# Kernel optimization log

Measured on AMD Instinct MI355X. Metric: run time of the kernel, lower is better.

The kernel has to match this reference:

```python
import jax, jax.numpy as jnp
import numpy as np

CUTOFF = 8.0
NUM_G = 50
HID = 128
NUM_INTER = 3
NUM_NODES = 50000
NUM_EDGES = 1600000
NUM_GRAPHS = 128
MAX_Z = 100
LOG2 = float(np.log(2.0))


def ssp(x):
    # PyG ShiftedSoftplus
    return jax.nn.softplus(x) - LOG2


def setup_inputs() -> dict:
    key = jax.random.key(0)
    ks = jax.random.split(key, 20)
    s = 0.1
    pos = jax.random.normal(ks[0], (NUM_NODES, 3), dtype=jnp.float32) * 4.0
    edge_shift = jax.random.normal(ks[1], (NUM_EDGES, 3), dtype=jnp.float32) * 0.5
    z = jax.random.randint(ks[2], (NUM_NODES,), 0, MAX_Z, dtype=jnp.int32)
    edge_index = jax.random.randint(ks[3], (2, NUM_EDGES), 0, NUM_NODES, dtype=jnp.int32)
    batch = jnp.sort(jax.random.randint(ks[4], (NUM_NODES,), 0, NUM_GRAPHS, dtype=jnp.int32))
    emb = jax.random.normal(ks[5], (MAX_Z, HID), dtype=jnp.float32) * s
    mlp_w1 = jax.random.normal(ks[6], (NUM_INTER, NUM_G, HID), dtype=jnp.float32) * s
    mlp_b1 = jnp.zeros((NUM_INTER, HID), jnp.float32)
    mlp_w2 = jax.random.normal(ks[7], (NUM_INTER, HID, HID), dtype=jnp.float32) * s
    mlp_b2 = jnp.zeros((NUM_INTER, HID), jnp.float32)
    cf_w1 = jax.random.normal(ks[8], (NUM_INTER, HID, HID), dtype=jnp.float32) * s  # no bias (PyG lin1)
    cf_w2 = jax.random.normal(ks[9], (NUM_INTER, HID, HID), dtype=jnp.float32) * s
    cf_b2 = jnp.zeros((NUM_INTER, HID), jnp.float32)
    lin_w = jax.random.normal(ks[10], (NUM_INTER, HID, HID), dtype=jnp.float32) * s
    lin_b = jnp.zeros((NUM_INTER, HID), jnp.float32)
    head_w1 = jax.random.normal(ks[11], (HID, HID // 2), dtype=jnp.float32) * s
    head_b1 = jnp.zeros((HID // 2,), jnp.float32)
    head_w2 = jax.random.normal(ks[12], (HID // 2, 1), dtype=jnp.float32) * s
    head_b2 = jnp.zeros((1,), jnp.float32)
    return dict(pos=pos, edge_shift=edge_shift, emb=emb, mlp_w1=mlp_w1, mlp_b1=mlp_b1,
                mlp_w2=mlp_w2, mlp_b2=mlp_b2, cf_w1=cf_w1, cf_w2=cf_w2, cf_b2=cf_b2,
                lin_w=lin_w, lin_b=lin_b, head_w1=head_w1, head_b1=head_b1,
                head_w2=head_w2, head_b2=head_b2, z=z, edge_index=edge_index, batch=batch)


def reference(pos, edge_shift, emb, mlp_w1, mlp_b1, mlp_w2, mlp_b2, cf_w1, cf_w2, cf_b2,
              lin_w, lin_b, head_w1, head_b1, head_w2, head_b2, z, edge_index, batch):
    src, dst = edge_index[0], edge_index[1]
    # edge distances: pos[row] - (pos[col] + shift)
    rel = pos[src] - (pos[dst] + edge_shift)            # [E,3]
    w = jnp.linalg.norm(rel, axis=-1)                   # [E]
    # Gaussian smearing
    offset = jnp.linspace(0.0, CUTOFF, NUM_G, dtype=pos.dtype)
    coeff = -0.5 / (offset[1] - offset[0]) ** 2
    edge_attr = jnp.exp(coeff * (w[:, None] - offset) ** 2)   # [E,50]
    # cosine cutoff
    C = 0.5 * (jnp.cos(w * jnp.pi / CUTOFF) + 1.0)            # [E]
    h = emb[z]                                                # [N,128]
    for i in range(NUM_INTER):
        Wf = (ssp(edge_attr @ mlp_w1[i] + mlp_b1[i]) @ mlp_w2[i] + mlp_b2[i]) * C[:, None]  # [E,128]
        msg = (h @ cf_w1[i])[src] * Wf                   # gather-multiply  [E,128]
        agg = jax.ops.segment_sum(msg, dst, num_segments=NUM_NODES)         # scatter-sum [N,128]
        h = h + (ssp(agg @ cf_w2[i] + cf_b2[i]) @ lin_w[i] + lin_b[i])
    out_atom = ssp(h @ head_w1 + head_b1) @ head_w2 + head_b2               # [N,1]
    sums = jax.ops.segment_sum(out_atom, batch, num_segments=NUM_GRAPHS)    # [G,1]
    counts = jax.ops.segment_sum(jnp.ones((NUM_NODES, 1), out_atom.dtype), batch, num_segments=NUM_GRAPHS)
    return sums / jnp.maximum(counts, 1.0)  # mean readout; out_proj is Identity (128==128)
```

## Files before the change

kernel.cpp:

```cpp
#include <hip/hip_runtime.h>
#include <hip/hip_fp16.h>
#include <math.h>

#define NNODES  50000
#define NEDGES  1600000
#define NGRAPHS 128
#define HID     128
#define NG      50
#define NITER   3
#define TPTS    2048
#define WMAX    12.0f
#define PI_F    3.14159265358979323846f

typedef __attribute__((ext_vector_type(4))) _Float16 half4;
typedef __attribute__((ext_vector_type(4))) float   f32x4;

__device__ __forceinline__ float ssp(float x) {
    float sp = fmaxf(x, 0.0f) + log1pf(expf(-fabsf(x)));
    return sp - 0.69314718055994530942f;
}

__global__ __launch_bounds__(256) void k_init_h(const float* __restrict__ emb,
                                                const int* __restrict__ z,
                                                float* __restrict__ h,
                                                _Float16* __restrict__ hH)
{
    int idx = blockIdx.x * 256 + threadIdx.x;
    int n = idx >> 7, c = idx & 127;
    float v = emb[(z[n] << 7) + c];
    h[idx] = v;
    hH[idx] = (_Float16)v;
}

__global__ __launch_bounds__(128) void k_wt(const float* __restrict__ in,
                                            _Float16* __restrict__ out)
{
    int it = blockIdx.x >> 7, c = blockIdx.x & 127, j = threadIdx.x;
    out[(size_t)it * 16384 + c * 128 + j] = (_Float16)in[(size_t)it * 16384 + j * 128 + c];
}

__global__ __launch_bounds__(128) void k_table(const float* __restrict__ W1,
                                               const float* __restrict__ B1,
                                               const float* __restrict__ W2,
                                               const float* __restrict__ B2,
                                               float* __restrict__ table)
{
    int it = blockIdx.x / TPTS;
    int pt = blockIdx.x - it * TPTS;
    const float* W1i = W1 + (size_t)it * NG * HID;
    const float* B1i = B1 + (size_t)it * HID;
    const float* W2i = W2 + (size_t)it * HID * HID;
    const float* B2i = B2 + (size_t)it * HID;

    float w = pt * (WMAX / (float)(TPTS - 1));
    __shared__ float sEA[NG];
    __shared__ float sT1[HID];
    int k = threadIdx.x;
    if (k < NG) {
        float dx = 8.0f / 49.0f;
        float coeff = -0.5f / (dx * dx);
        float diff = w - (float)k * dx;
        sEA[k] = expf(coeff * diff * diff);
    }
    __syncthreads();
    float acc = B1i[k];
    for (int g = 0; g < NG; ++g) acc = fmaf(sEA[g], W1i[g * HID + k], acc);
    sT1[k] = ssp(acc);
    __syncthreads();
    float acc2 = B2i[k];
    for (int j = 0; j < HID; ++j) acc2 = fmaf(sT1[j], W2i[j * HID + k], acc2);
    table[(size_t)blockIdx.x * HID + k] = acc2;
}

__global__ __launch_bounds__(256) void k_tdelta(const float* __restrict__ raw,
                                                __half* __restrict__ ti)
{
    int idx = blockIdx.x * 256 + threadIdx.x;
    int c = idx & 127;
    int pt_it = idx >> 7;
    int pt = pt_it & (TPTS - 1);
    float v = raw[idx];
    float nv = (pt == TPTS - 1) ? v : raw[idx + HID];
    ti[(size_t)pt_it * 256 + c * 2]     = __float2half(v);
    ti[(size_t)pt_it * 256 + c * 2 + 1] = __float2half(nv - v);
}

__global__ __launch_bounds__(256) void k_hist(const int* __restrict__ ei,
                                              int* __restrict__ deg)
{
    int e = blockIdx.x * 256 + threadIdx.x;
    if (e >= NEDGES) return;
    atomicAdd(&deg[ei[NEDGES + e]], 1);
}

#define SCAN_T 1024
#define CHUNK  49
__global__ __launch_bounds__(SCAN_T) void k_scan(const int* __restrict__ deg,
                                                 int* __restrict__ rowptr,
                                                 int* __restrict__ cursor)
{
    int tid = threadIdx.x;
    int base = tid * CHUNK;
    int vals[CHUNK];
    int local = 0;
    #pragma unroll
    for (int i = 0; i < CHUNK; ++i) {
        int idx = base + i;
        int v = (idx < NNODES) ? deg[idx] : 0;
        vals[i] = local;
        local += v;
    }
    int lane = tid & 63, wid = tid >> 6;
    int x = local;
    #pragma unroll
    for (int off = 1; off < 64; off <<= 1) {
        int y = __shfl_up(x, off);
        if (lane >= off) x += y;
    }
    __shared__ int wsum[16];
    __shared__ int woff[17];
    if (lane == 63) wsum[wid] = x;
    __syncthreads();
    if (tid == 0) {
        int acc = 0;
        #pragma unroll
        for (int i = 0; i < 16; ++i) { woff[i] = acc; acc += wsum[i]; }
        woff[16] = acc;
    }
    __syncthreads();
    int threadExcl = woff[wid] + x - local;
    #pragma unroll
    for (int i = 0; i < CHUNK; ++i) {
        int idx = base + i;
        if (idx < NNODES) {
            int p = threadExcl + vals[i];
            rowptr[idx] = p;
            cursor[idx] = p;
        }
    }
    if (tid == SCAN_T - 1) rowptr[NNODES] = woff[16];
}

__global__ __launch_bounds__(256) void k_scatter(const int* __restrict__ ei,
                                                 const float* __restrict__ pos,
                                                 const float* __restrict__ shift,
                                                 int* __restrict__ cursor,
                                                 float2* __restrict__ rec)
{
    int e = blockIdx.x * 256 + threadIdx.x;
    if (e >= NEDGES) return;
    int s = ei[e], d = ei[NEDGES + e];
    float rx = pos[3*s+0] - (pos[3*d+0] + shift[3*e+0]);
    float ry = pos[3*s+1] - (pos[3*d+1] + shift[3*e+1]);
    float rz = pos[3*s+2] - (pos[3*d+2] + shift[3*e+2]);
    float w = sqrtf(rx*rx + ry*ry + rz*rz);
    int slot = atomicAdd(&cursor[d], 1);
    rec[slot] = make_float2(__int_as_float(s), w);
}

__device__ __forceinline__ void edge_contrib(float2 r, int lane,
                                             const __half2* __restrict__ hfH,
                                             const __half* __restrict__ tableH,
                                             float& ax, float& ay)
{
    int   s = __float_as_int(r.x);
    float w = r.y;
    const float SCALE = (float)(TPTS - 1) / WMAX;
    float t = fminf(w * SCALE, (float)(TPTS - 1));
    int i0 = (int)t; if (i0 > TPTS - 2) i0 = TPTS - 2;
    float fr = t - (float)i0;
    float C = 0.5f * (__cosf(w * (PI_F / 8.0f)) + 1.0f);
    uint2 tv = *((const uint2*)(tableH + (size_t)i0 * 256) + lane);
    __half2 hv = hfH[(size_t)s * 64 + lane];
    float2 p0 = __half22float2(*(__half2*)&tv.x);
    float2 p1 = __half22float2(*(__half2*)&tv.y);
    float2 hf2 = __half22float2(hv);
    ax = fmaf(fmaf(fr, p0.y, p0.x) * C, hf2.x, ax);
    ay = fmaf(fmaf(fr, p1.y, p1.x) * C, hf2.y, ay);
}

__global__ __launch_bounds__(256) void k_gather(const float2* __restrict__ rec,
                                                const int* __restrict__ rowptr,
                                                const __half2* __restrict__ hfH,
                                                const __half* __restrict__ tableH,
                                                __half2* __restrict__ aggH)
{
    int node = blockIdx.x * 4 + (threadIdx.x >> 6);
    int lane = threadIdx.x & 63;
    int beg = rowptr[node], end = rowptr[node + 1];
    float ax0 = 0.f, ay0 = 0.f, ax1 = 0.f, ay1 = 0.f;
    int k = beg;
    for (; k + 4 <= end; k += 4) {
        float2 r0 = rec[k];
        float2 r1 = rec[k + 1];
        float2 r2 = rec[k + 2];
        float2 r3 = rec[k + 3];
        edge_contrib(r0, lane, hfH, tableH, ax0, ay0);
        edge_contrib(r1, lane, hfH, tableH, ax1, ay1);
        edge_contrib(r2, lane, hfH, tableH, ax0, ay0);
        edge_contrib(r3, lane, hfH, tableH, ax1, ay1);
    }
    for (; k < end; ++k) {
        float2 r0 = rec[k];
        edge_contrib(r0, lane, hfH, tableH, ax0, ay0);
    }
    aggH[(size_t)node * 64 + lane] = __floats2half2_rn(ax0 + ax1, ay0 + ay1);
}

__global__ __launch_bounds__(256) void k_ngemm_mfma(const _Float16* __restrict__ hH,
                                                    const _Float16* __restrict__ Wt,
                                                    _Float16* __restrict__ outH)
{
    int tid = threadIdx.x;
    int wave = tid >> 6, l = tid & 63;
    int lr = l & 15, lg = l >> 4;
    int r0 = blockIdx.x * 64 + wave * 16;
    f32x4 acc[8];
    #pragma unroll
    for (int ct = 0; ct < 8; ++ct) acc[ct] = (f32x4){0.f, 0.f, 0.f, 0.f};
    const _Float16* aRow = hH + (size_t)(r0 + lr) * HID;
    #pragma unroll
    for (int kk = 0; kk < 8; ++kk) {
        half4 a = *(const half4*)(aRow + kk * 16 + lg * 4);
        #pragma unroll
        for (int ct = 0; ct < 8; ++ct) {
            half4 b = *(const half4*)(Wt + (size_t)(ct * 16 + lr) * HID + kk * 16 + lg * 4);
            acc[ct] = __builtin_amdgcn_mfma_f32_16x16x16f16(a, b, acc[ct], 0, 0, 0);
        }
    }
    #pragma unroll
    for (int ct = 0; ct < 8; ++ct) {
        #pragma unroll
        for (int r = 0; r < 4; ++r) {
            int row = r0 + lg * 4 + r;
            if (row < NNODES) outH[(size_t)row * HID + ct * 16 + lr] = (_Float16)acc[ct][r];
        }
    }
}

__global__ __launch_bounds__(256) void k_update_mfma(const _Float16* __restrict__ aggH,
                                                     const _Float16* __restrict__ W2t,
                                                     const float* __restrict__ B2,
                                                     const _Float16* __restrict__ Lt,
                                                     const float* __restrict__ LB,
                                                     float* __restrict__ h,
                                                     _Float16* __restrict__ hH)
{
    __shared__ _Float16 sT[64 * 128];
    int tid = threadIdx.x;
    int wave = tid >> 6, l = tid & 63;
    int lr = l & 15, lg = l >> 4;
    int r0 = blockIdx.x * 64 + wave * 16;

    f32x4 acc[8];
    #pragma unroll
    for (int ct = 0; ct < 8; ++ct) acc[ct] = (f32x4){0.f, 0.f, 0.f, 0.f};
    const _Float16* aRow = aggH + (size_t)(r0 + lr) * HID;
    #pragma unroll
    for (int kk = 0; kk < 8; ++kk) {
        half4 a = *(const half4*)(aRow + kk * 16 + lg * 4);
        #pragma unroll
        for (int ct = 0; ct < 8; ++ct) {
            half4 b = *(const half4*)(W2t + (size_t)(ct * 16 + lr) * HID + kk * 16 + lg * 4);
            acc[ct] = __builtin_amdgcn_mfma_f32_16x16x16f16(a, b, acc[ct], 0, 0, 0);
        }
    }
    #pragma unroll
    for (int ct = 0; ct < 8; ++ct) {
        #pragma unroll
        for (int r = 0; r < 4; ++r) {
            int rl = wave * 16 + lg * 4 + r;
            int col = ct * 16 + lr;
            float v = ssp(acc[ct][r] + B2[col]);
            int byte = rl * 256 + col * 2;
            byte ^= (rl & 7) << 4;
            *(_Float16*)((char*)sT + byte) = (_Float16)v;
        }
    }
    __syncthreads();
    f32x4 acc2[8];
    #pragma unroll
    for (int ct = 0; ct < 8; ++ct) acc2[ct] = (f32x4){0.f, 0.f, 0.f, 0.f};
    int rl2 = wave * 16 + lr;
    #pragma unroll
    for (int kk = 0; kk < 8; ++kk) {
        int byte = rl2 * 256 + (kk * 16 + lg * 4) * 2;
        byte ^= (rl2 & 7) << 4;
        half4 a = *(const half4*)((char*)sT + byte);
        #pragma unroll
        for (int ct = 0; ct < 8; ++ct) {
            half4 b = *(const half4*)(Lt + (size_t)(ct * 16 + lr) * HID + kk * 16 + lg * 4);
            acc2[ct] = __builtin_amdgcn_mfma_f32_16x16x16f16(a, b, acc2[ct], 0, 0, 0);
        }
    }
    #pragma unroll
    for (int ct = 0; ct < 8; ++ct) {
        #pragma unroll
        for (int r = 0; r < 4; ++r) {
            int row = r0 + lg * 4 + r;
            int col = ct * 16 + lr;
            if (row < NNODES) {
                float hv = h[(size_t)row * HID + col] + acc2[ct][r] + LB[col];
                h[(size_t)row * HID + col] = hv;
                hH[(size_t)row * HID + col] = (_Float16)hv;
            }
        }
    }
}

__global__ __launch_bounds__(512) void k_head(const float* __restrict__ h,
                                              const float* __restrict__ w1,
                                              const float* __restrict__ b1,
                                              const float* __restrict__ w2,
                                              const float* __restrict__ b2,
                                              const int* __restrict__ batch,
                                              float* __restrict__ sums_pad)
{
    __shared__ float sA[128 * 132];
    int r0 = blockIdx.x * 128;
    int tid = threadIdx.x;
    for (int idx = tid; idx < 128 * 32; idx += 512) {
        int r = idx >> 5, c4 = idx & 31;
        int row = r0 + r;
        float4 v = make_float4(0.f, 0.f, 0.f, 0.f);
        if (row < NNODES) v = *(const float4*)(h + (size_t)row * HID + c4 * 4);
        *(float4*)(&sA[r * 132 + c4 * 4]) = v;
    }
    __syncthreads();
    int tx = tid & 7, ty = tid >> 3;
    int cc = tx * 8, ee = ty * 2;
    float acc[2][8];
    {
        float4 b0 = *(const float4*)(b1 + cc);
        float4 bb = *(const float4*)(b1 + cc + 4);
        #pragma unroll
        for (int e = 0; e < 2; ++e) {
            acc[e][0]=b0.x; acc[e][1]=b0.y; acc[e][2]=b0.z; acc[e][3]=b0.w;
            acc[e][4]=bb.x; acc[e][5]=bb.y; acc[e][6]=bb.z; acc[e][7]=bb.w;
        }
    }
    #pragma unroll 4
    for (int j = 0; j < HID; ++j) {
        float a0 = sA[(ee + 0) * 132 + j];
        float a1 = sA[(ee + 1) * 132 + j];
        float4 w0 = *(const float4*)(w1 + (size_t)j * 64 + cc);
        float4 wv1 = *(const float4*)(w1 + (size_t)j * 64 + cc + 4);
        float wv[8] = {w0.x,w0.y,w0.z,w0.w,wv1.x,wv1.y,wv1.z,wv1.w};
        #pragma unroll
        for (int c = 0; c < 8; ++c) {
            acc[0][c] = fmaf(a0, wv[c], acc[0][c]);
            acc[1][c] = fmaf(a1, wv[c], acc[1][c]);
        }
    }
    float4 w2a = *(const float4*)(w2 + cc);
    float4 w2b = *(const float4*)(w2 + cc + 4);
    float w2v[8] = {w2a.x,w2a.y,w2a.z,w2a.w,w2b.x,w2b.y,w2b.z,w2b.w};
    float bias2 = b2[0];
    #pragma unroll
    for (int e = 0; e < 2; ++e) {
        float part = 0.f;
        #pragma unroll
        for (int c = 0; c < 8; ++c) part = fmaf(ssp(acc[e][c]), w2v[c], part);
        part += __shfl_down(part, 4, 8);
        part += __shfl_down(part, 2, 8);
        part += __shfl_down(part, 1, 8);
        if (tx == 0) {
            int row = r0 + ee + e;
            if (row < NNODES) {
                int b = batch[row];
                atomicAdd(&sums_pad[b * 16], part + bias2);
            }
        }
    }
}

__global__ void k_final(const float* __restrict__ sums_pad,
                        const int* __restrict__ batch,
                        float* __restrict__ out)
{
    int g = threadIdx.x;
    if (g >= NGRAPHS) return;
    int lo = 0, hi = NNODES;
    while (lo < hi) { int mid = (lo + hi) >> 1; if (batch[mid] < g) lo = mid + 1; else hi = mid; }
    int a = lo;
    lo = 0; hi = NNODES;
    while (lo < hi) { int mid = (lo + hi) >> 1; if (batch[mid] < g + 1) lo = mid + 1; else hi = mid; }
    float cnt = (float)(lo - a);
    out[g] = sums_pad[g * 16] / fmaxf(cnt, 1.0f);
}

extern "C" void kernel_launch(void* const* d_in, const int* in_sizes, int n_in,
                              void* d_out, int out_size, void* d_ws, size_t ws_size,
                              hipStream_t stream)
{
    const float* pos     = (const float*)d_in[0];
    const float* shift   = (const float*)d_in[1];
    const float* emb     = (const float*)d_in[2];
    const float* mlp_w1  = (const float*)d_in[3];
    const float* mlp_b1  = (const float*)d_in[4];
    const float* mlp_w2  = (const float*)d_in[5];
    const float* mlp_b2  = (const float*)d_in[6];
    const float* cf_w1   = (const float*)d_in[7];
    const float* cf_w2   = (const float*)d_in[8];
    const float* cf_b2   = (const float*)d_in[9];
    const float* lin_w   = (const float*)d_in[10];
    const float* lin_b   = (const float*)d_in[11];
    const float* head_w1 = (const float*)d_in[12];
    const float* head_b1 = (const float*)d_in[13];
    const float* head_w2 = (const float*)d_in[14];
    const float* head_b2 = (const float*)d_in[15];
    const int*   z       = (const int*)d_in[16];
    const int*   ei      = (const int*)d_in[17];
    const int*   batch   = (const int*)d_in[18];
    float* out = (float*)d_out;

    float* ws = (float*)d_ws;
    size_t off = 0;
    float*    h       = ws + off; off += (size_t)NNODES * HID;
    _Float16* hH      = (_Float16*)(ws + off); off += (size_t)(NNODES + 64) * HID / 2;
    _Float16* hfH     = (_Float16*)(ws + off); off += (size_t)(NNODES + 64) * HID / 2;
    _Float16* aggH    = (_Float16*)(ws + off); off += (size_t)(NNODES + 64) * HID / 2;
    float*    rawT    = ws + off; off += (size_t)3 * TPTS * HID;
    __half*   tableH  = (__half*)(ws + off); off += (size_t)3 * TPTS * HID;
    _Float16* w1t     = (_Float16*)(ws + off); off += (size_t)3 * HID * HID / 2;
    _Float16* w2t     = (_Float16*)(ws + off); off += (size_t)3 * HID * HID / 2;
    _Float16* lwt     = (_Float16*)(ws + off); off += (size_t)3 * HID * HID / 2;
    float2*   rec     = (float2*)(ws + off); off += (size_t)2 * NEDGES;
    int*      rowptr  = (int*)(ws + off); off += NNODES + 1;
    int*      deg     = (int*)(ws + off); off += NNODES;
    int*      cursor  = (int*)(ws + off); off += NNODES;
    float*    sums_pad= ws + off; off += NGRAPHS * 16;

    hipMemsetAsync(deg, 0, NNODES * sizeof(int), stream);
    hipMemsetAsync(sums_pad, 0, NGRAPHS * 16 * sizeof(float), stream);

    k_hist<<<(NEDGES + 255) / 256, 256, 0, stream>>>(ei, deg);
    k_scan<<<1, SCAN_T, 0, stream>>>(deg, rowptr, cursor);
    k_scatter<<<(NEDGES + 255) / 256, 256, 0, stream>>>(ei, pos, shift, cursor, rec);

    k_init_h<<<NNODES * HID / 256, 256, 0, stream>>>(emb, z, h, hH);
    k_table<<<3 * TPTS, 128, 0, stream>>>(mlp_w1, mlp_b1, mlp_w2, mlp_b2, rawT);
    k_tdelta<<<(3 * TPTS * HID) / 256, 256, 0, stream>>>(rawT, tableH);
    k_wt<<<3 * 128, 128, 0, stream>>>(cf_w1, w1t);
    k_wt<<<3 * 128, 128, 0, stream>>>(cf_w2, w2t);
    k_wt<<<3 * 128, 128, 0, stream>>>(lin_w, lwt);

    int gblk = (NNODES + 63) / 64;
    for (int i = 0; i < NITER; ++i) {
        k_ngemm_mfma<<<gblk, 256, 0, stream>>>(hH, w1t + (size_t)i * HID * HID, hfH);
        k_gather<<<NNODES / 4, 256, 0, stream>>>(rec, rowptr, (const __half2*)hfH,
                                                 tableH + (size_t)i * TPTS * HID * 2,
                                                 (__half2*)aggH);
        k_update_mfma<<<gblk, 256, 0, stream>>>(aggH, w2t + (size_t)i * HID * HID,
                                                cf_b2 + (size_t)i * HID,
                                                lwt + (size_t)i * HID * HID,
                                                lin_b + (size_t)i * HID, h, hH);
    }
    k_head<<<(NNODES + 127) / 128, 512, 0, stream>>>(h, head_w1, head_b1, head_w2, head_b2, batch, sums_pad);
    k_final<<<1, 128, 0, stream>>>(sums_pad, batch, out);
}
```

Before: 1.051 ms.

## Precompute per-edge table offsets, fuse next-layer GEMM into update, merge table kernels

The scatter kernel now stores a 16-byte record per edge holding the pre-scaled source offset, table offset, interpolation fraction and cutoff value in fp16. This moves the index, fraction and cosine work out of the gather kernel that runs three times. The gather uses readfirstlane scalar offsets and half2 arithmetic. The update kernel also computes the next iteration's h@cf_w1 through MFMA from its shared-memory tile, which removes two separate node-GEMM launches and their hH reload. The table kernel writes interleaved fp16 values and deltas directly, dropping the tdelta pass. In exchange the edge record doubles in size, raising gather read traffic, and fp16 math adds rounding.

```diff
diff --git a/kernel.cpp b/kernel.cpp
--- a/kernel.cpp
+++ b/kernel.cpp
@@ -43,7 +43,7 @@
                                                const float* __restrict__ B1,
                                                const float* __restrict__ W2,
                                                const float* __restrict__ B2,
-                                               float* __restrict__ table)
+                                               __half* __restrict__ ti)
 {
     int it = blockIdx.x / TPTS;
     int pt = blockIdx.x - it * TPTS;
@@ -52,37 +52,45 @@
     const float* W2i = W2 + (size_t)it * HID * HID;
     const float* B2i = B2 + (size_t)it * HID;
 
-    float w = pt * (WMAX / (float)(TPTS - 1));
-    __shared__ float sEA[NG];
-    __shared__ float sT1[HID];
+    const float step = WMAX / (float)(TPTS - 1);
+    float w0 = pt * step;
+    int ptn = (pt < TPTS - 1) ? pt + 1 : pt;
+    float w1v = ptn * step;
+
+    __shared__ float sEA[2][NG];
+    __shared__ float sT1[2][HID];
     int k = threadIdx.x;
-    if (k < NG) {
+    {
         float dx = 8.0f / 49.0f;
         float coeff = -0.5f / (dx * dx);
-        float diff = w - (float)k * dx;
-        sEA[k] = expf(coeff * diff * diff);
-    }
-    __syncthreads();
-    float acc = B1i[k];
-    for (int g = 0; g < NG; ++g) acc = fmaf(sEA[g], W1i[g * HID + k], acc);
-    sT1[k] = ssp(acc);
-    __syncthreads();
-    float acc2 = B2i[k];
-    for (int j = 0; j < HID; ++j) acc2 = fmaf(sT1[j], W2i[j * HID + k], acc2);
-    table[(size_t)blockIdx.x * HID + k] = acc2;
-}
-
-__global__ __launch_bounds__(256) void k_tdelta(const float* __restrict__ raw,
-                                                __half* __restrict__ ti)
-{
-    int idx = blockIdx.x * 256 + threadIdx.x;
-    int c = idx & 127;
-    int pt_it = idx >> 7;
-    int pt = pt_it & (TPTS - 1);
-    float v = raw[idx];
-    float nv = (pt == TPTS - 1) ? v : raw[idx + HID];
-    ti[(size_t)pt_it * 256 + c * 2]     = __float2half(v);
-    ti[(size_t)pt_it * 256 + c * 2 + 1] = __float2half(nv - v);
+        if (k < NG) {
+            float diff = w0 - (float)k * dx;
+            sEA[0][k] = expf(coeff * diff * diff);
+        } else if (k >= 64 && k < 64 + NG) {
+            float diff = w1v - (float)(k - 64) * dx;
+            sEA[1][k - 64] = expf(coeff * diff * diff);
+        }
+    }
+    __syncthreads();
+    float a0 = B1i[k], a1 = a0;
+    for (int g = 0; g < NG; ++g) {
+        float wv = W1i[g * HID + k];
+        a0 = fmaf(sEA[0][g], wv, a0);
+        a1 = fmaf(sEA[1][g], wv, a1);
+    }
+    sT1[0][k] = ssp(a0);
+    sT1[1][k] = ssp(a1);
+    __syncthreads();
+    float b0 = B2i[k], b1v = b0;
+    for (int j = 0; j < HID; ++j) {
+        float wv = W2i[j * HID + k];
+        b0  = fmaf(sT1[0][j], wv, b0);
+        b1v = fmaf(sT1[1][j], wv, b1v);
+    }
+    size_t base = ((size_t)it * TPTS + pt) * 256;
+    int pair = k >> 1, within = k & 1;
+    ti[base + pair * 4 + within]     = __float2half(b0);
+    ti[base + pair * 4 + within + 2] = __float2half(b1v - b0);
 }
 
 __global__ __launch_bounds__(256) void k_hist(const int* __restrict__ ei,
@@ -145,7 +153,7 @@
                                                  const float* __restrict__ pos,
                                                  const float* __restrict__ shift,
                                                  int* __restrict__ cursor,
-                                                 float2* __restrict__ rec)
+                                                 uint4* __restrict__ rec)
 {
     int e = blockIdx.x * 256 + threadIdx.x;
     if (e >= NEDGES) return;
@@ -154,56 +162,60 @@
     float ry = pos[3*s+1] - (pos[3*d+1] + shift[3*e+1]);
     float rz = pos[3*s+2] - (pos[3*d+2] + shift[3*e+2]);
     float w = sqrtf(rx*rx + ry*ry + rz*rz);
-    int slot = atomicAdd(&cursor[d], 1);
-    rec[slot] = make_float2(__int_as_float(s), w);
-}
-
-__device__ __forceinline__ void edge_contrib(float2 r, int lane,
-                                             const __half2* __restrict__ hfH,
-                                             const __half* __restrict__ tableH,
-                                             float& ax, float& ay)
-{
-    int   s = __float_as_int(r.x);
-    float w = r.y;
     const float SCALE = (float)(TPTS - 1) / WMAX;
     float t = fminf(w * SCALE, (float)(TPTS - 1));
     int i0 = (int)t; if (i0 > TPTS - 2) i0 = TPTS - 2;
     float fr = t - (float)i0;
-    float C = 0.5f * (__cosf(w * (PI_F / 8.0f)) + 1.0f);
-    uint2 tv = *((const uint2*)(tableH + (size_t)i0 * 256) + lane);
-    __half2 hv = hfH[(size_t)s * 64 + lane];
-    float2 p0 = __half22float2(*(__half2*)&tv.x);
-    float2 p1 = __half22float2(*(__half2*)&tv.y);
-    float2 hf2 = __half22float2(hv);
-    ax = fmaf(fmaf(fr, p0.y, p0.x) * C, hf2.x, ax);
-    ay = fmaf(fmaf(fr, p1.y, p1.x) * C, hf2.y, ay);
-}
-
-__global__ __launch_bounds__(256) void k_gather(const float2* __restrict__ rec,
+    float C = 0.5f * (cosf(w * (PI_F / 8.0f)) + 1.0f);
+    __half2 fr2 = __float2half2_rn(fr);
+    __half2 c2  = __float2half2_rn(C);
+    int slot = atomicAdd(&cursor[d], 1);
+    rec[slot] = make_uint4((unsigned)(s * 256), (unsigned)(i0 * 512),
+                           *(unsigned*)&fr2, *(unsigned*)&c2);
+}
+
+__device__ __forceinline__ void edge_contrib(uint4 rv,
+                                             const char* __restrict__ hfLane,
+                                             const char* __restrict__ tbLane,
+                                             float& ax, float& ay)
+{
+    int srcB = __builtin_amdgcn_readfirstlane((int)rv.x);
+    int tblO = __builtin_amdgcn_readfirstlane((int)rv.y);
+    int fru  = __builtin_amdgcn_readfirstlane((int)rv.z);
+    int cu   = __builtin_amdgcn_readfirstlane((int)rv.w);
+    __half2 fr2 = *reinterpret_cast<__half2*>(&fru);
+    __half2 c2  = *reinterpret_cast<__half2*>(&cu);
+    uint2 tv = *reinterpret_cast<const uint2*>(tbLane + tblO);
+    __half2 hv = *reinterpret_cast<const __half2*>(hfLane + srcB);
+    __half2 vals = *reinterpret_cast<__half2*>(&tv.x);
+    __half2 dels = *reinterpret_cast<__half2*>(&tv.y);
+    __half2 f2 = __hfma2(fr2, dels, vals);
+    __half2 ch = __hmul2(c2, hv);
+    ax = fmaf(__low2float(f2),  __low2float(ch),  ax);
+    ay = fmaf(__high2float(f2), __high2float(ch), ay);
+}
+
+__global__ __launch_bounds__(256) void k_gather(const uint4* __restrict__ rec,
                                                 const int* __restrict__ rowptr,
-                                                const __half2* __restrict__ hfH,
+                                                const __half* __restrict__ hfH,
                                                 const __half* __restrict__ tableH,
                                                 __half2* __restrict__ aggH)
 {
     int node = blockIdx.x * 4 + (threadIdx.x >> 6);
     int lane = threadIdx.x & 63;
+    const char* hfLane = (const char*)hfH + lane * 4;
+    const char* tbLane = (const char*)tableH + lane * 8;
     int beg = rowptr[node], end = rowptr[node + 1];
     float ax0 = 0.f, ay0 = 0.f, ax1 = 0.f, ay1 = 0.f;
     int k = beg;
     for (; k + 4 <= end; k += 4) {
-        float2 r0 = rec[k];
-        float2 r1 = rec[k + 1];
-        float2 r2 = rec[k + 2];
-        float2 r3 = rec[k + 3];
-        edge_contrib(r0, lane, hfH, tableH, ax0, ay0);
-        edge_contrib(r1, lane, hfH, tableH, ax1, ay1);
-        edge_contrib(r2, lane, hfH, tableH, ax0, ay0);
-        edge_contrib(r3, lane, hfH, tableH, ax1, ay1);
-    }
-    for (; k < end; ++k) {
-        float2 r0 = rec[k];
-        edge_contrib(r0, lane, hfH, tableH, ax0, ay0);
-    }
+        uint4 r0 = rec[k], r1 = rec[k+1], r2 = rec[k+2], r3 = rec[k+3];
+        edge_contrib(r0, hfLane, tbLane, ax0, ay0);
+        edge_contrib(r1, hfLane, tbLane, ax1, ay1);
+        edge_contrib(r2, hfLane, tbLane, ax0, ay0);
+        edge_contrib(r3, hfLane, tbLane, ax1, ay1);
+    }
+    for (; k < end; ++k) edge_contrib(rec[k], hfLane, tbLane, ax0, ay0);
     aggH[(size_t)node * 64 + lane] = __floats2half2_rn(ax0 + ax1, ay0 + ay1);
 }
 
@@ -244,7 +256,9 @@
                                                      const _Float16* __restrict__ Lt,
                                                      const float* __restrict__ LB,
                                                      float* __restrict__ h,
-                                                     _Float16* __restrict__ hH)
+                                                     _Float16* __restrict__ hH,
+                                                     const _Float16* __restrict__ W1n,
+                                                     _Float16* __restrict__ hfOut)
 {
     __shared__ _Float16 sT[64 * 128];
     int tid = threadIdx.x;
@@ -293,16 +307,49 @@
             acc2[ct] = __builtin_amdgcn_mfma_f32_16x16x16f16(a, b, acc2[ct], 0, 0, 0);
         }
     }
+    __syncthreads();
     #pragma unroll
     for (int ct = 0; ct < 8; ++ct) {
         #pragma unroll
         for (int r = 0; r < 4; ++r) {
             int row = r0 + lg * 4 + r;
             int col = ct * 16 + lr;
+            float hv = 0.f;
             if (row < NNODES) {
-                float hv = h[(size_t)row * HID + col] + acc2[ct][r] + LB[col];
+                hv = h[(size_t)row * HID + col] + acc2[ct][r] + LB[col];
                 h[(size_t)row * HID + col] = hv;
                 hH[(size_t)row * HID + col] = (_Float16)hv;
+            }
+            if (W1n) {
+                int rl = wave * 16 + lg * 4 + r;
+                int byte = rl * 256 + col * 2;
+                byte ^= (rl & 7) << 4;
+                *(_Float16*)((char*)sT + byte) = (_Float16)hv;
+            }
+        }
+    }
+    if (W1n) {
+        __syncthreads();
+        f32x4 acc3[8];
+        #pragma unroll
+        for (int ct = 0; ct < 8; ++ct) acc3[ct] = (f32x4){0.f, 0.f, 0.f, 0.f};
+        #pragma unroll
+        for (int kk = 0; kk < 8; ++kk) {
+            int byte = rl2 * 256 + (kk * 16 + lg * 4) * 2;
+            byte ^= (rl2 & 7) << 4;
+            half4 a = *(const half4*)((char*)sT + byte);
+            #pragma unroll
+            for (int ct = 0; ct < 8; ++ct) {
+                half4 b = *(const half4*)(W1n + (size_t)(ct * 16 + lr) * HID + kk * 16 + lg * 4);
+                acc3[ct] = __builtin_amdgcn_mfma_f32_16x16x16f16(a, b, acc3[ct], 0, 0, 0);
+            }
+        }
+        #pragma unroll
+        for (int ct = 0; ct < 8; ++ct) {
+            #pragma unroll
+            for (int r = 0; r < 4; ++r) {
+                int row = r0 + lg * 4 + r;
+                if (row < NNODES) hfOut[(size_t)row * HID + ct * 16 + lr] = (_Float16)acc3[ct][r];
             }
         }
     }
@@ -420,12 +467,11 @@
     _Float16* hH      = (_Float16*)(ws + off); off += (size_t)(NNODES + 64) * HID / 2;
     _Float16* hfH     = (_Float16*)(ws + off); off += (size_t)(NNODES + 64) * HID / 2;
     _Float16* aggH    = (_Float16*)(ws + off); off += (size_t)(NNODES + 64) * HID / 2;
-    float*    rawT    = ws + off; off += (size_t)3 * TPTS * HID;
-    __half*   tableH  = (__half*)(ws + off); off += (size_t)3 * TPTS * HID;
+    __half*   tableH  = (__half*)(ws + off); off += (size_t)3 * TPTS * 256 / 2;
     _Float16* w1t     = (_Float16*)(ws + off); off += (size_t)3 * HID * HID / 2;
     _Float16* w2t     = (_Float16*)(ws + off); off += (size_t)3 * HID * HID / 2;
     _Float16* lwt     = (_Float16*)(ws + off); off += (size_t)3 * HID * HID / 2;
-    float2*   rec     = (float2*)(ws + off); off += (size_t)2 * NEDGES;
+    uint4*    rec     = (uint4*)(ws + off); off += (size_t)4 * NEDGES;
     int*      rowptr  = (int*)(ws + off); off += NNODES + 1;
     int*      deg     = (int*)(ws + off); off += NNODES;
     int*      cursor  = (int*)(ws + off); off += NNODES;
@@ -439,22 +485,23 @@
     k_scatter<<<(NEDGES + 255) / 256, 256, 0, stream>>>(ei, pos, shift, cursor, rec);
 
     k_init_h<<<NNODES * HID / 256, 256, 0, stream>>>(emb, z, h, hH);
-    k_table<<<3 * TPTS, 128, 0, stream>>>(mlp_w1, mlp_b1, mlp_w2, mlp_b2, rawT);
-    k_tdelta<<<(3 * TPTS * HID) / 256, 256, 0, stream>>>(rawT, tableH);
+    k_table<<<3 * TPTS, 128, 0, stream>>>(mlp_w1, mlp_b1, mlp_w2, mlp_b2, tableH);
     k_wt<<<3 * 128, 128, 0, stream>>>(cf_w1, w1t);
     k_wt<<<3 * 128, 128, 0, stream>>>(cf_w2, w2t);
     k_wt<<<3 * 128, 128, 0, stream>>>(lin_w, lwt);
 
     int gblk = (NNODES + 63) / 64;
+    k_ngemm_mfma<<<gblk, 256, 0, stream>>>(hH, w1t, hfH);
     for (int i = 0; i < NITER; ++i) {
-        k_ngemm_mfma<<<gblk, 256, 0, stream>>>(hH, w1t + (size_t)i * HID * HID, hfH);
-        k_gather<<<NNODES / 4, 256, 0, stream>>>(rec, rowptr, (const __half2*)hfH,
-                                                 tableH + (size_t)i * TPTS * HID * 2,
+        k_gather<<<NNODES / 4, 256, 0, stream>>>(rec, rowptr, (const __half*)hfH,
+                                                 tableH + (size_t)i * TPTS * 256,
                                                  (__half2*)aggH);
         k_update_mfma<<<gblk, 256, 0, stream>>>(aggH, w2t + (size_t)i * HID * HID,
                                                 cf_b2 + (size_t)i * HID,
                                                 lwt + (size_t)i * HID * HID,
-                                                lin_b + (size_t)i * HID, h, hH);
+                                                lin_b + (size_t)i * HID, h, hH,
+                                                (i < NITER - 1) ? w1t + (size_t)(i + 1) * HID * HID : nullptr,
+                                                hfH);
     }
     k_head<<<(NNODES + 127) / 128, 512, 0, stream>>>(h, head_w1, head_b1, head_w2, head_b2, batch, sums_pad);
     k_final<<<1, 128, 0, stream>>>(sums_pad, batch, out);
```

Measured after the change: 1.170 ms. 11.3% more time.
